# Optimization experiments

Hardware: AMD Instinct MI355X
Metric: run time of the kernel (lower is better)

## Reference

```python
import jax, jax.numpy as jnp
import numpy as np

SFREQ = 250.0
L_FREQ, H_FREQ = 4.0, 8.0
N_TAPS = 413  # odd, zero-phase 'auto' length for 2 Hz transition band at 250 Hz


def _bandpass_fir(numtaps, f1, f2, sfreq):
    # hamming-windowed firwin band-pass (stand-in for mne.create_filter output)
    m = np.arange(numtaps) - (numtaps - 1) / 2.0
    h = (2.0 * f2 / sfreq) * np.sinc(2.0 * f2 / sfreq * m) \
        - (2.0 * f1 / sfreq) * np.sinc(2.0 * f1 / sfreq * m)
    h = h * np.hamming(numtaps)
    return h.astype(np.float32)


def setup_inputs() -> dict:
    key = jax.random.key(0)
    x = jax.random.normal(key, (32, 64, 30000), dtype=jnp.float32)
    h = jnp.asarray(_bandpass_fir(N_TAPS, L_FREQ, H_FREQ, SFREQ))
    return {"x": x, "h": h}


def reference(x, h):
    # Vectorized overlap-add FIR filtering == one full FFT linear convolution
    # of the reflect_limited-padded signal, then centered (zero-phase) slice.
    B, C, T = x.shape
    n_h = h.shape[0]
    n_edge = min(n_h, T) - 1          # smart-pad width on each edge
    xf = x.reshape(-1, T)             # (B*C, T)
    # reflect_limited padding: 2*x[0] - x[n_edge:0:-1]  /  2*x[-1] - x[-2:-n_edge-2:-1]
    left = 2.0 * xf[:, :1] - xf[:, 1:n_edge + 1][:, ::-1]
    right = 2.0 * xf[:, -1:] - xf[:, -n_edge - 1:-1][:, ::-1]
    x_ext = jnp.concatenate([left, xf, right], axis=1)  # (B*C, T + 2*n_edge)
    n_x = T + 2 * n_edge
    n_fft = n_x + n_h - 1             # full linear convolution length
    X = jnp.fft.rfft(x_ext, n=n_fft, axis=1)
    H = jnp.fft.rfft(h, n=n_fft)
    y = jnp.fft.irfft(X * H[None, :], n=n_fft, axis=1)   # conv_full(x_ext, h)
    shift = (n_h - 1) // 2 + n_edge   # zero-phase group-delay + edge compensation
    out = jax.lax.dynamic_slice_in_dim(y, shift, T, axis=1)
    return out.reshape(B, C, T).astype(x.dtype)
```

## Files before the change

### kernel.cpp

```cpp
#include <hip/hip_runtime.h>


#define T_LEN   30000
#define NTAPS   413
#define BLOCK   256
#define OUT_BLK 2048
#define BLK_PER_SIG 15
#define NSIG_A  14
#define XS_LEN  2480
#define NCHUNK  310
#define LDS_CHUNKS 348

typedef __bf16 bf16x8 __attribute__((ext_vector_type(8)));
typedef float  f32x4  __attribute__((ext_vector_type(4)));

union Chunk {
    uint4 v;
    unsigned short us[8];
    bf16x8 f;
};

__device__ __forceinline__ unsigned short f32_to_bf16_rne(float f) {
    unsigned u = __float_as_uint(f);
    unsigned r = u + 0x7FFFu + ((u >> 16) & 1u);
    return (unsigned short)(r >> 16);
}

__device__ __forceinline__ int cpad(int u) { return u + (u >> 3); }

__global__ void prep_A_kernel(const float* __restrict__ h, uint4* __restrict__ wsA) {
    int i = blockIdx.x * blockDim.x + threadIdx.x;
    if (i >= NSIG_A * 64) return;
    int sig = i >> 6, lane = i & 63;
    int r = lane & 15, q = lane >> 4;
    Chunk c;
    #pragma unroll
    for (int j = 0; j < 8; ++j) {
        int idx = 430 + r - 8 * q - j - 32 * sig;
        float v = (idx >= 0 && idx < NTAPS) ? h[idx] : 0.0f;
        c.us[j] = f32_to_bf16_rne(v);
    }
    wsA[i] = c.v;
}

__global__ __launch_bounds__(BLOCK, 4) void fir_mfma_kernel(
    const float* __restrict__ x, const uint4* __restrict__ wsA,
    float* __restrict__ out)
{
    __shared__ uint4 lds[LDS_CHUNKS];

    const int tid = threadIdx.x;
    const int sig_id = blockIdx.x / BLK_PER_SIG;
    const int blk    = blockIdx.x % BLK_PER_SIG;
    const int t0 = blk * OUT_BLK;
    const float* xp = x   + (size_t)sig_id * T_LEN;
    float*       op = out + (size_t)sig_id * T_LEN;

    const int lane = tid & 63;
    const int wv   = tid >> 6;
    bf16x8 A[NSIG_A];
    #pragma unroll
    for (int s = 0; s < NSIG_A; ++s) {
        Chunk c; c.v = wsA[s * 64 + lane];
        A[s] = c.f;
    }

    for (int u = tid; u < NCHUNK; u += BLOCK) {
        int g0 = t0 - 224 + 8 * u;
        Chunk c;
        if (g0 >= 0 && g0 + 8 <= T_LEN) {
            float4 a = *reinterpret_cast<const float4*>(xp + g0);
            float4 b = *reinterpret_cast<const float4*>(xp + g0 + 4);
            c.us[0] = f32_to_bf16_rne(a.x); c.us[1] = f32_to_bf16_rne(a.y);
            c.us[2] = f32_to_bf16_rne(a.z); c.us[3] = f32_to_bf16_rne(a.w);
            c.us[4] = f32_to_bf16_rne(b.x); c.us[5] = f32_to_bf16_rne(b.y);
            c.us[6] = f32_to_bf16_rne(b.z); c.us[7] = f32_to_bf16_rne(b.w);
        } else {
            float x0 = xp[0], xl = xp[T_LEN - 1];
            #pragma unroll
            for (int j = 0; j < 8; ++j) {
                int g = g0 + j;
                float v;
                if (g < 0)            v = 2.0f * x0 - xp[-g];
                else if (g >= T_LEN)  v = 2.0f * xl - xp[2 * T_LEN - 2 - g];
                else                  v = xp[g];
                c.us[j] = f32_to_bf16_rne(v);
            }
        }
        lds[cpad(u)] = c.v;
    }
    __syncthreads();

    const int n = lane & 15, q = lane >> 4;
    const int base_u = 64 * wv + 2 * n + q;

    f32x4 acc0 = {0.f, 0.f, 0.f, 0.f};
    f32x4 acc1 = {0.f, 0.f, 0.f, 0.f};

    #pragma unroll
    for (int phi = 0; phi < NSIG_A + 8; ++phi) {
        int u = base_u + 4 * phi;
        Chunk c; c.v = lds[cpad(u)];
        bf16x8 B = c.f;
        if (phi < NSIG_A)
            acc0 = __builtin_amdgcn_mfma_f32_16x16x32_bf16(A[phi], B, acc0, 0, 0, 0);
        if (phi >= 8)
            acc1 = __builtin_amdgcn_mfma_f32_16x16x32_bf16(A[phi - 8], B, acc1, 0, 0, 0);
    }

    const int tA = t0 + 256 * (2 * wv) + 16 * n + 4 * q;
    if (tA < T_LEN)
        *reinterpret_cast<float4*>(op + tA) = make_float4(acc0.x, acc0.y, acc0.z, acc0.w);
    const int tB = tA + 256;
    if (tB < T_LEN)
        *reinterpret_cast<float4*>(op + tB) = make_float4(acc1.x, acc1.y, acc1.z, acc1.w);
}

extern "C" void kernel_launch(void* const* d_in, const int* in_sizes, int n_in,
                              void* d_out, int out_size, void* d_ws, size_t ws_size,
                              hipStream_t stream) {
    const float* x = (const float*)d_in[0];
    const float* h = (const float*)d_in[1];
    float* out = (float*)d_out;
    uint4* wsA = (uint4*)d_ws;
    const int nsig = in_sizes[0] / T_LEN;

    prep_A_kernel<<<dim3(4), dim3(BLOCK), 0, stream>>>(h, wsA);
    fir_mfma_kernel<<<dim3(nsig * BLK_PER_SIG), dim3(BLOCK), 0, stream>>>(x, wsA, out);
}
```

Before: 435.8 us.

## Process whole signal per block with double-buffered LDS prefetch

Each block now handles one whole signal, looping over its 15 output tiles instead of launching one block per tile. The global loads for the next tile are issued into registers before the MFMA work on the current tile, then converted and stored into the second LDS buffer, so memory latency overlaps with compute. The cost is a much smaller grid (2048 blocks instead of 30720), which means less parallelism and load balance across CUs, plus longer per-block serial chains and extra registers held for the prefetched data.

```diff
diff --git a/kernel.cpp b/kernel.cpp
--- a/kernel.cpp
+++ b/kernel.cpp
@@ -43,21 +43,56 @@
     wsA[i] = c.v;
 }
 
+__device__ __forceinline__ void chunk_load(const float* __restrict__ xp, int g0,
+                                           float r[8]) {
+    if (g0 >= 0 && g0 + 8 <= T_LEN) {
+        float4 a = *reinterpret_cast<const float4*>(xp + g0);
+        float4 b = *reinterpret_cast<const float4*>(xp + g0 + 4);
+        r[0] = a.x; r[1] = a.y; r[2] = a.z; r[3] = a.w;
+        r[4] = b.x; r[5] = b.y; r[6] = b.z; r[7] = b.w;
+    } else {
+        #pragma unroll
+        for (int j = 0; j < 8; ++j) {
+            int g = g0 + j;
+            int idx = (g < 0) ? -g : ((g >= T_LEN) ? (2 * T_LEN - 2 - g) : g);
+            r[j] = xp[idx];
+        }
+    }
+}
+
+__device__ __forceinline__ void chunk_store(uint4* __restrict__ buf, int u, int g0,
+                                            const float r[8], float x0, float xl) {
+    Chunk c;
+    if (g0 >= 0 && g0 + 8 <= T_LEN) {
+        #pragma unroll
+        for (int j = 0; j < 8; ++j) c.us[j] = f32_to_bf16_rne(r[j]);
+    } else {
+        #pragma unroll
+        for (int j = 0; j < 8; ++j) {
+            int g = g0 + j;
+            float v = r[j];
+            if (g < 0)           v = 2.0f * x0 - v;
+            else if (g >= T_LEN) v = 2.0f * xl - v;
+            c.us[j] = f32_to_bf16_rne(v);
+        }
+    }
+    buf[cpad(u)] = c.v;
+}
+
 __global__ __launch_bounds__(BLOCK, 4) void fir_mfma_kernel(
     const float* __restrict__ x, const uint4* __restrict__ wsA,
     float* __restrict__ out)
 {
-    __shared__ uint4 lds[LDS_CHUNKS];
+    __shared__ uint4 lds[2][LDS_CHUNKS];
 
     const int tid = threadIdx.x;
-    const int sig_id = blockIdx.x / BLK_PER_SIG;
-    const int blk    = blockIdx.x % BLK_PER_SIG;
-    const int t0 = blk * OUT_BLK;
+    const int sig_id = blockIdx.x;
     const float* xp = x   + (size_t)sig_id * T_LEN;
     float*       op = out + (size_t)sig_id * T_LEN;
 
     const int lane = tid & 63;
     const int wv   = tid >> 6;
+
     bf16x8 A[NSIG_A];
     #pragma unroll
     for (int s = 0; s < NSIG_A; ++s) {
@@ -65,55 +100,63 @@
         A[s] = c.f;
     }
 
-    for (int u = tid; u < NCHUNK; u += BLOCK) {
-        int g0 = t0 - 224 + 8 * u;
-        Chunk c;
-        if (g0 >= 0 && g0 + 8 <= T_LEN) {
-            float4 a = *reinterpret_cast<const float4*>(xp + g0);
-            float4 b = *reinterpret_cast<const float4*>(xp + g0 + 4);
-            c.us[0] = f32_to_bf16_rne(a.x); c.us[1] = f32_to_bf16_rne(a.y);
-            c.us[2] = f32_to_bf16_rne(a.z); c.us[3] = f32_to_bf16_rne(a.w);
-            c.us[4] = f32_to_bf16_rne(b.x); c.us[5] = f32_to_bf16_rne(b.y);
-            c.us[6] = f32_to_bf16_rne(b.z); c.us[7] = f32_to_bf16_rne(b.w);
-        } else {
-            float x0 = xp[0], xl = xp[T_LEN - 1];
-            #pragma unroll
-            for (int j = 0; j < 8; ++j) {
-                int g = g0 + j;
-                float v;
-                if (g < 0)            v = 2.0f * x0 - xp[-g];
-                else if (g >= T_LEN)  v = 2.0f * xl - xp[2 * T_LEN - 2 - g];
-                else                  v = xp[g];
-                c.us[j] = f32_to_bf16_rne(v);
-            }
-        }
-        lds[cpad(u)] = c.v;
+    const float x0 = xp[0], xl = xp[T_LEN - 1];
+
+    const bool has2 = (tid < NCHUNK - 256);
+    float r0[8], r1[8];
+
+    {
+        int g0 = -224 + 8 * tid;
+        chunk_load(xp, g0, r0);
+        if (has2) chunk_load(xp, g0 + 8 * 256, r1);
+        chunk_store(&lds[0][0], tid, g0, r0, x0, xl);
+        if (has2) chunk_store(&lds[0][0], tid + 256, g0 + 8 * 256, r1, x0, xl);
     }
     __syncthreads();
 
     const int n = lane & 15, q = lane >> 4;
     const int base_u = 64 * wv + 2 * n + q;
 
-    f32x4 acc0 = {0.f, 0.f, 0.f, 0.f};
-    f32x4 acc1 = {0.f, 0.f, 0.f, 0.f};
+    for (int blk = 0; blk < BLK_PER_SIG; ++blk) {
+        const int cur = blk & 1;
+        const int t0  = blk * OUT_BLK;
+        const bool pf = (blk + 1 < BLK_PER_SIG);
+        const int ng0 = (blk + 1) * OUT_BLK - 224 + 8 * tid;
 
-    #pragma unroll
-    for (int phi = 0; phi < NSIG_A + 8; ++phi) {
-        int u = base_u + 4 * phi;
-        Chunk c; c.v = lds[cpad(u)];
-        bf16x8 B = c.f;
-        if (phi < NSIG_A)
-            acc0 = __builtin_amdgcn_mfma_f32_16x16x32_bf16(A[phi], B, acc0, 0, 0, 0);
-        if (phi >= 8)
-            acc1 = __builtin_amdgcn_mfma_f32_16x16x32_bf16(A[phi - 8], B, acc1, 0, 0, 0);
+        if (pf) {
+            chunk_load(xp, ng0, r0);
+            if (has2) chunk_load(xp, ng0 + 8 * 256, r1);
+        }
+
+        const uint4* __restrict__ cb = &lds[cur][0];
+        f32x4 acc0 = {0.f, 0.f, 0.f, 0.f};
+        f32x4 acc1 = {0.f, 0.f, 0.f, 0.f};
+        #pragma unroll
+        for (int phi = 0; phi < NSIG_A + 8; ++phi) {
+            Chunk c; c.v = cb[cpad(base_u + 4 * phi)];
+            bf16x8 B = c.f;
+            if (phi < NSIG_A)
+                acc0 = __builtin_amdgcn_mfma_f32_16x16x32_bf16(A[phi], B, acc0, 0, 0, 0);
+            if (phi >= 8)
+                acc1 = __builtin_amdgcn_mfma_f32_16x16x32_bf16(A[phi - 8], B, acc1, 0, 0, 0);
+        }
+
+        const int tA = t0 + 256 * (2 * wv) + 16 * n + 4 * q;
+        if (tA < T_LEN)
+            *reinterpret_cast<float4*>(op + tA) =
+                make_float4(acc0.x, acc0.y, acc0.z, acc0.w);
+        const int tB = tA + 256;
+        if (tB < T_LEN)
+            *reinterpret_cast<float4*>(op + tB) =
+                make_float4(acc1.x, acc1.y, acc1.z, acc1.w);
+
+        if (pf) {
+            uint4* __restrict__ nb = &lds[cur ^ 1][0];
+            chunk_store(nb, tid, ng0, r0, x0, xl);
+            if (has2) chunk_store(nb, tid + 256, ng0 + 8 * 256, r1, x0, xl);
+        }
+        __syncthreads();
     }
-
-    const int tA = t0 + 256 * (2 * wv) + 16 * n + 4 * q;
-    if (tA < T_LEN)
-        *reinterpret_cast<float4*>(op + tA) = make_float4(acc0.x, acc0.y, acc0.z, acc0.w);
-    const int tB = tA + 256;
-    if (tB < T_LEN)
-        *reinterpret_cast<float4*>(op + tB) = make_float4(acc1.x, acc1.y, acc1.z, acc1.w);
 }
 
 extern "C" void kernel_launch(void* const* d_in, const int* in_sizes, int n_in,
@@ -126,5 +169,5 @@
     const int nsig = in_sizes[0] / T_LEN;
 
     prep_A_kernel<<<dim3(4), dim3(BLOCK), 0, stream>>>(h, wsA);
-    fir_mfma_kernel<<<dim3(nsig * BLK_PER_SIG), dim3(BLOCK), 0, stream>>>(x, wsA, out);
+    fir_mfma_kernel<<<dim3(nsig), dim3(BLOCK), 0, stream>>>(x, wsA, out);
 }
```

Result: no change. 437.4 us (+0.4%).

## Use 32x32x16 MFMA and loop persistent blocks over signal tiles

Applied to the files above, without the earlier changes.

Switches the Toeplitz-style FIR matmul from 16x16x32 MFMA with two accumulators to a single 32x32x16 bf16 MFMA chain over 28 filter-tap blocks. Each workgroup now owns a whole signal and loops over 8 output tiles of 4096 samples, with the last tile overlapped so stores need no bounds checks. This loads the filter A fragments once per signal instead of once per 2048-sample block. In exchange there are fewer workgroups (one per signal), higher register pressure (occupancy bound lowered to 3) and two barriers per tile with no overlap between staging and compute.

```diff
diff --git a/kernel.cpp b/kernel.cpp
--- a/kernel.cpp
+++ b/kernel.cpp
@@ -4,15 +4,15 @@
 #define T_LEN   30000
 #define NTAPS   413
 #define BLOCK   256
-#define OUT_BLK 2048
-#define BLK_PER_SIG 15
-#define NSIG_A  14
-#define XS_LEN  2480
-#define NCHUNK  310
-#define LDS_CHUNKS 348
+#define OUT_BLK 4096
+#define NTILE   8
+#define LAST_T0 25904
+#define NSIG    28
+#define NCHUNK3 564
+#define LDS_PHYS 704
 
 typedef __bf16 bf16x8 __attribute__((ext_vector_type(8)));
-typedef float  f32x4  __attribute__((ext_vector_type(4)));
+typedef float  f32x16 __attribute__((ext_vector_type(16)));
 
 union Chunk {
     uint4 v;
@@ -26,94 +26,101 @@
     return (unsigned short)(r >> 16);
 }
 
-__device__ __forceinline__ int cpad(int u) { return u + (u >> 3); }
+__device__ __forceinline__ int cpad2(int u) { return u + (u >> 2); }
 
 __global__ void prep_A_kernel(const float* __restrict__ h, uint4* __restrict__ wsA) {
     int i = blockIdx.x * blockDim.x + threadIdx.x;
-    if (i >= NSIG_A * 64) return;
+    if (i >= NSIG * 64) return;
     int sig = i >> 6, lane = i & 63;
-    int r = lane & 15, q = lane >> 4;
+    int r = lane & 31, b = lane >> 5;
     Chunk c;
     #pragma unroll
     for (int j = 0; j < 8; ++j) {
-        int idx = 430 + r - 8 * q - j - 32 * sig;
+        int idx = 414 + r - 8 * b - j - 16 * sig;
         float v = (idx >= 0 && idx < NTAPS) ? h[idx] : 0.0f;
         c.us[j] = f32_to_bf16_rne(v);
     }
     wsA[i] = c.v;
 }
 
-__global__ __launch_bounds__(BLOCK, 4) void fir_mfma_kernel(
+__device__ __forceinline__ void stage_chunk(uint4* __restrict__ buf,
+                                            const float* __restrict__ xp,
+                                            int u, int s0) {
+    int g0 = s0 + 8 * u;
+    Chunk c;
+    if (g0 >= 0 && g0 + 8 <= T_LEN) {
+        float4 a = *reinterpret_cast<const float4*>(xp + g0);
+        float4 b = *reinterpret_cast<const float4*>(xp + g0 + 4);
+        c.us[0] = f32_to_bf16_rne(a.x); c.us[1] = f32_to_bf16_rne(a.y);
+        c.us[2] = f32_to_bf16_rne(a.z); c.us[3] = f32_to_bf16_rne(a.w);
+        c.us[4] = f32_to_bf16_rne(b.x); c.us[5] = f32_to_bf16_rne(b.y);
+        c.us[6] = f32_to_bf16_rne(b.z); c.us[7] = f32_to_bf16_rne(b.w);
+    } else {
+        float x0 = xp[0], xl = xp[T_LEN - 1];
+        #pragma unroll
+        for (int j = 0; j < 8; ++j) {
+            int g = g0 + j;
+            float v;
+            if (g < 0)            v = 2.0f * x0 - xp[-g];
+            else if (g >= T_LEN)  v = 2.0f * xl - xp[2 * T_LEN - 2 - g];
+            else                  v = xp[g];
+            c.us[j] = f32_to_bf16_rne(v);
+        }
+    }
+    buf[cpad2(u)] = c.v;
+}
+
+__global__ __launch_bounds__(BLOCK, 3) void fir_mfma_kernel(
     const float* __restrict__ x, const uint4* __restrict__ wsA,
     float* __restrict__ out)
 {
-    __shared__ uint4 lds[LDS_CHUNKS];
+    __shared__ uint4 lds[LDS_PHYS];
 
-    const int tid = threadIdx.x;
-    const int sig_id = blockIdx.x / BLK_PER_SIG;
-    const int blk    = blockIdx.x % BLK_PER_SIG;
-    const int t0 = blk * OUT_BLK;
+    const int tid  = threadIdx.x;
+    const int lane = tid & 63;
+    const int wv   = tid >> 6;
+    const int sig_id = blockIdx.x;
     const float* xp = x   + (size_t)sig_id * T_LEN;
     float*       op = out + (size_t)sig_id * T_LEN;
 
-    const int lane = tid & 63;
-    const int wv   = tid >> 6;
-    bf16x8 A[NSIG_A];
+    bf16x8 A[NSIG];
     #pragma unroll
-    for (int s = 0; s < NSIG_A; ++s) {
+    for (int s = 0; s < NSIG; ++s) {
         Chunk c; c.v = wsA[s * 64 + lane];
         A[s] = c.f;
     }
 
-    for (int u = tid; u < NCHUNK; u += BLOCK) {
-        int g0 = t0 - 224 + 8 * u;
-        Chunk c;
-        if (g0 >= 0 && g0 + 8 <= T_LEN) {
-            float4 a = *reinterpret_cast<const float4*>(xp + g0);
-            float4 b = *reinterpret_cast<const float4*>(xp + g0 + 4);
-            c.us[0] = f32_to_bf16_rne(a.x); c.us[1] = f32_to_bf16_rne(a.y);
-            c.us[2] = f32_to_bf16_rne(a.z); c.us[3] = f32_to_bf16_rne(a.w);
-            c.us[4] = f32_to_bf16_rne(b.x); c.us[5] = f32_to_bf16_rne(b.y);
-            c.us[6] = f32_to_bf16_rne(b.z); c.us[7] = f32_to_bf16_rne(b.w);
-        } else {
-            float x0 = xp[0], xl = xp[T_LEN - 1];
-            #pragma unroll
-            for (int j = 0; j < 8; ++j) {
-                int g = g0 + j;
-                float v;
-                if (g < 0)            v = 2.0f * x0 - xp[-g];
-                else if (g >= T_LEN)  v = 2.0f * xl - xp[2 * T_LEN - 2 - g];
-                else                  v = xp[g];
-                c.us[j] = f32_to_bf16_rne(v);
-            }
+    const int c31 = lane & 31;
+    const int kb  = lane >> 5;
+    const int ub  = 128 * wv + 4 * c31 + kb;
+
+    for (int blk = 0; blk < NTILE; ++blk) {
+        const int t0 = (blk < NTILE - 1) ? blk * OUT_BLK : LAST_T0;
+        const int s0 = t0 - 208;
+
+        stage_chunk(lds, xp, tid, s0);
+        stage_chunk(lds, xp, tid + 256, s0);
+        if (tid < NCHUNK3 - 512) stage_chunk(lds, xp, tid + 512, s0);
+        __syncthreads();
+
+        f32x16 acc = {0.f, 0.f, 0.f, 0.f, 0.f, 0.f, 0.f, 0.f,
+                      0.f, 0.f, 0.f, 0.f, 0.f, 0.f, 0.f, 0.f};
+        #pragma unroll
+        for (int sg = 0; sg < NSIG; ++sg) {
+            Chunk ch; ch.v = lds[cpad2(ub + 2 * sg)];
+            acc = __builtin_amdgcn_mfma_f32_32x32x16_bf16(A[sg], ch.f, acc, 0, 0, 0);
         }
-        lds[cpad(u)] = c.v;
+
+        const int tb   = t0 + 1024 * wv;
+        const int tcol = tb + 32 * c31 + 4 * kb;
+        #pragma unroll
+        for (int g = 0; g < 4; ++g) {
+            *reinterpret_cast<float4*>(op + tcol + 8 * g) =
+                make_float4(acc[4 * g + 0], acc[4 * g + 1],
+                            acc[4 * g + 2], acc[4 * g + 3]);
+        }
+        __syncthreads();
     }
-    __syncthreads();
-
-    const int n = lane & 15, q = lane >> 4;
-    const int base_u = 64 * wv + 2 * n + q;
-
-    f32x4 acc0 = {0.f, 0.f, 0.f, 0.f};
-    f32x4 acc1 = {0.f, 0.f, 0.f, 0.f};
-
-    #pragma unroll
-    for (int phi = 0; phi < NSIG_A + 8; ++phi) {
-        int u = base_u + 4 * phi;
-        Chunk c; c.v = lds[cpad(u)];
-        bf16x8 B = c.f;
-        if (phi < NSIG_A)
-            acc0 = __builtin_amdgcn_mfma_f32_16x16x32_bf16(A[phi], B, acc0, 0, 0, 0);
-        if (phi >= 8)
-            acc1 = __builtin_amdgcn_mfma_f32_16x16x32_bf16(A[phi - 8], B, acc1, 0, 0, 0);
-    }
-
-    const int tA = t0 + 256 * (2 * wv) + 16 * n + 4 * q;
-    if (tA < T_LEN)
-        *reinterpret_cast<float4*>(op + tA) = make_float4(acc0.x, acc0.y, acc0.z, acc0.w);
-    const int tB = tA + 256;
-    if (tB < T_LEN)
-        *reinterpret_cast<float4*>(op + tB) = make_float4(acc1.x, acc1.y, acc1.z, acc1.w);
 }
 
 extern "C" void kernel_launch(void* const* d_in, const int* in_sizes, int n_in,
@@ -125,6 +132,6 @@
     uint4* wsA = (uint4*)d_ws;
     const int nsig = in_sizes[0] / T_LEN;
 
-    prep_A_kernel<<<dim3(4), dim3(BLOCK), 0, stream>>>(h, wsA);
-    fir_mfma_kernel<<<dim3(nsig * BLK_PER_SIG), dim3(BLOCK), 0, stream>>>(x, wsA, out);
+    prep_A_kernel<<<dim3(7), dim3(BLOCK), 0, stream>>>(h, wsA);
+    fir_mfma_kernel<<<dim3(nsig), dim3(BLOCK), 0, stream>>>(x, wsA, out);
 }
```

After: 488.5 us. +12.1%, slower.
